# Optimization experiments

Measured on AMD Instinct MI355X. Metric: run time of the kernel, lower is better.

## Reference

```python
import jax, jax.numpy as jnp
import numpy as np

N_NODES = 100000
N_EDGES = 1600000
IN = 128
HID = 128
EPS = 1e-5


def setup_inputs() -> dict:
    key = jax.random.key(0)
    ks = jax.random.split(key, 20)
    def lin(k, fi, fo):
        return jax.random.normal(k, (fi, fo), dtype=jnp.float32) / np.sqrt(fi)
    inp = {
        'x': jax.random.normal(ks[0], (N_NODES, IN), dtype=jnp.float32),
        'src': jax.random.randint(ks[1], (N_EDGES,), 0, N_NODES),
        'dst': jax.random.randint(ks[2], (N_EDGES,), 0, N_NODES),
        # SAGEConv layer 1..3: fc_self, fc_neigh, bias
        'Wself1': lin(ks[3], IN, HID), 'Wneigh1': lin(ks[4], IN, HID), 'b1': jnp.zeros((HID,), jnp.float32),
        'Wself2': lin(ks[5], HID, HID), 'Wneigh2': lin(ks[6], HID, HID), 'b2': jnp.zeros((HID,), jnp.float32),
        'Wself3': lin(ks[7], HID, HID), 'Wneigh3': lin(ks[8], HID, HID), 'b3': jnp.zeros((HID,), jnp.float32),
        # shared BatchNorm1d(hid)
        'gamma': jnp.ones((HID,), jnp.float32), 'beta': jnp.zeros((HID,), jnp.float32),
        # decoder MLP hid->hid->hid->1
        'Wd1': lin(ks[9], HID, HID), 'bd1': jnp.zeros((HID,), jnp.float32),
        'Wd2': lin(ks[10], HID, HID), 'bd2': jnp.zeros((HID,), jnp.float32),
        'Wd3': lin(ks[11], HID, 1), 'bd3': jnp.zeros((1,), jnp.float32),
    }
    return inp


def _sage_conv(h, src, dst, deg, Wself, Wneigh, b, n):
    # mean aggregation over in-neighbors: gather + segment-sum + divide
    neigh_sum = jax.ops.segment_sum(h[src], dst, num_segments=n)  # [N, F]
    neigh_mean = neigh_sum / deg[:, None]
    return h @ Wself + neigh_mean @ Wneigh + b


def _batch_norm(h, gamma, beta):
    mu = jnp.mean(h, axis=0)
    var = jnp.mean(jnp.square(h - mu), axis=0)  # biased var, as torch BN training
    return gamma * (h - mu) * jax.lax.rsqrt(var + EPS) + beta


def reference(x, src, dst, Wself1, Wneigh1, b1, Wself2, Wneigh2, b2,
              Wself3, Wneigh3, b3, gamma, beta, Wd1, bd1, Wd2, bd2, Wd3, bd3):
    n = x.shape[0]
    deg = jax.ops.segment_sum(jnp.ones_like(dst, dtype=x.dtype), dst, num_segments=n)
    deg = jnp.maximum(deg, 1.0)
    h = _sage_conv(x, src, dst, deg, Wself1, Wneigh1, b1, n)
    h = jax.nn.relu(_batch_norm(h, gamma, beta))  # dropout = identity (eval)
    h = _sage_conv(h, src, dst, deg, Wself2, Wneigh2, b2, n)
    h = jax.nn.relu(_batch_norm(h, gamma, beta))
    h = _sage_conv(h, src, dst, deg, Wself3, Wneigh3, b3, n)
    # decoder MLP
    h = jax.nn.relu(h @ Wd1 + bd1)
    h = jax.nn.relu(h @ Wd2 + bd2)
    return h @ Wd3 + bd3  # [N, 1]
```

## Files before the change

### kernel.cpp

```cpp
#include <hip/hip_runtime.h>

typedef unsigned short u16;
typedef unsigned int u32;
using bf16x8 = __attribute__((ext_vector_type(8))) __bf16;
using f32x4  = __attribute__((ext_vector_type(4))) float;

#define CAP 48

__global__ void SAGE_79328045957727_kernel() {}

__device__ __forceinline__ float bf2f(u16 u) {
  union { u32 i; float f; } v; v.i = ((u32)u) << 16; return v.f;
}
__device__ __forceinline__ u16 f2bf(float f) {
  union { float f; u32 i; } v; v.f = f;
  u32 x = v.i;
  return (u16)((x + 0x7FFFu + ((x >> 16) & 1u)) >> 16);
}


__global__ void zero_kernel(int* p, int n) {
  int i = blockIdx.x * 256 + threadIdx.x;
  if (i < n) p[i] = 0;
}

__global__ void f32_to_bf16_kernel(const float* in, u16* out, long n) {
  long i = (long)blockIdx.x * 256 + threadIdx.x;
  if (i < n) out[i] = f2bf(in[i]);
}

__global__ void transpose_all_kernel(
    const float* w0, const float* w1, const float* w2, const float* w3,
    const float* w4, const float* w5, const float* w6, const float* w7,
    u16* wt) {
  int m = blockIdx.x >> 6;
  const float* W = m == 0 ? w0 : m == 1 ? w1 : m == 2 ? w2 : m == 3 ? w3
                 : m == 4 ? w4 : m == 5 ? w5 : m == 6 ? w6 : w7;
  u16* Wt = wt + (size_t)m * 16384;
  int i = (blockIdx.x & 63) * 256 + threadIdx.x;
  int r = i >> 7, c = i & 127;
  Wt[(size_t)c * 128 + r] = f2bf(W[(size_t)r * 128 + c]);
}


__global__ __launch_bounds__(256) void scatter_pad_kernel(
    const int* __restrict__ src, const int* __restrict__ dst,
    int* __restrict__ deg, int* __restrict__ csr, int E, int npart) {
  int p = blockIdx.x & 7;
  int brank = blockIdx.x >> 3;
  int bpp = gridDim.x >> 3;
  int lo = p * npart, hi = lo + npart;
  for (int i = brank * 256 + threadIdx.x; i < E; i += bpp * 256) {
    int dv = dst[i];
    if (dv >= lo && dv < hi) {
      int pos = atomicAdd(&deg[dv], 1);
      if (pos < CAP) csr[(size_t)dv * CAP + pos] = src[i];
    }
  }
}


__global__ __launch_bounds__(256) void gather_mean_kernel(
    const u16* __restrict__ H, const int* __restrict__ csr,
    const int* __restrict__ deg, u16* __restrict__ M, int N) {
  int node = blockIdx.x * 16 + (threadIdx.x >> 4);
  if (node >= N) return;
  int lane = threadIdx.x & 15;
  int fo = lane * 8;
  const int* nl = csr + (size_t)node * CAP;
  int d = deg[node];
  int dm = d < CAP ? d : CAP;
  float a0=0.f,a1=0.f,a2=0.f,a3=0.f,a4=0.f,a5=0.f,a6=0.f,a7=0.f;
  int e = 0;
  for (; e + 4 <= dm; e += 4) {
    int i0 = nl[e];
    int i1 = nl[e + 1];
    int i2 = nl[e + 2];
    int i3 = nl[e + 3];
    uint4 q0 = *(const uint4*)(H + (size_t)i0 * 128 + fo);
    uint4 q1 = *(const uint4*)(H + (size_t)i1 * 128 + fo);
    uint4 q2 = *(const uint4*)(H + (size_t)i2 * 128 + fo);
    uint4 q3 = *(const uint4*)(H + (size_t)i3 * 128 + fo);
    a0 += bf2f((u16)(q0.x & 0xffffu)); a1 += bf2f((u16)(q0.x >> 16));
    a2 += bf2f((u16)(q0.y & 0xffffu)); a3 += bf2f((u16)(q0.y >> 16));
    a4 += bf2f((u16)(q0.z & 0xffffu)); a5 += bf2f((u16)(q0.z >> 16));
    a6 += bf2f((u16)(q0.w & 0xffffu)); a7 += bf2f((u16)(q0.w >> 16));
    a0 += bf2f((u16)(q1.x & 0xffffu)); a1 += bf2f((u16)(q1.x >> 16));
    a2 += bf2f((u16)(q1.y & 0xffffu)); a3 += bf2f((u16)(q1.y >> 16));
    a4 += bf2f((u16)(q1.z & 0xffffu)); a5 += bf2f((u16)(q1.z >> 16));
    a6 += bf2f((u16)(q1.w & 0xffffu)); a7 += bf2f((u16)(q1.w >> 16));
    a0 += bf2f((u16)(q2.x & 0xffffu)); a1 += bf2f((u16)(q2.x >> 16));
    a2 += bf2f((u16)(q2.y & 0xffffu)); a3 += bf2f((u16)(q2.y >> 16));
    a4 += bf2f((u16)(q2.z & 0xffffu)); a5 += bf2f((u16)(q2.z >> 16));
    a6 += bf2f((u16)(q2.w & 0xffffu)); a7 += bf2f((u16)(q2.w >> 16));
    a0 += bf2f((u16)(q3.x & 0xffffu)); a1 += bf2f((u16)(q3.x >> 16));
    a2 += bf2f((u16)(q3.y & 0xffffu)); a3 += bf2f((u16)(q3.y >> 16));
    a4 += bf2f((u16)(q3.z & 0xffffu)); a5 += bf2f((u16)(q3.z >> 16));
    a6 += bf2f((u16)(q3.w & 0xffffu)); a7 += bf2f((u16)(q3.w >> 16));
  }
  for (; e < dm; ++e) {
    int s = nl[e];
    uint4 q = *(const uint4*)(H + (size_t)s * 128 + fo);
    a0 += bf2f((u16)(q.x & 0xffffu)); a1 += bf2f((u16)(q.x >> 16));
    a2 += bf2f((u16)(q.y & 0xffffu)); a3 += bf2f((u16)(q.y >> 16));
    a4 += bf2f((u16)(q.z & 0xffffu)); a5 += bf2f((u16)(q.z >> 16));
    a6 += bf2f((u16)(q.w & 0xffffu)); a7 += bf2f((u16)(q.w >> 16));
  }
  float inv = 1.f / (float)(d > 0 ? d : 1);
  uint4 o;
  o.x = ((u32)f2bf(a1 * inv) << 16) | (u32)f2bf(a0 * inv);
  o.y = ((u32)f2bf(a3 * inv) << 16) | (u32)f2bf(a2 * inv);
  o.z = ((u32)f2bf(a5 * inv) << 16) | (u32)f2bf(a4 * inv);
  o.w = ((u32)f2bf(a7 * inv) << 16) | (u32)f2bf(a6 * inv);
  *(uint4*)(M + (size_t)node * 128 + fo) = o;
}


#define LDSROW 136

template <int DUAL, int RELU, int STATS>
__global__ __launch_bounds__(256) void gemm_mfma(
    const u16* __restrict__ A, const u16* __restrict__ B,
    const u16* __restrict__ W1t, const u16* __restrict__ W2t,
    const float* __restrict__ bias, u16* __restrict__ C,
    float* __restrict__ stats, int N) {
  __shared__ u16 sT[128 * LDSROW];

  int tid = threadIdx.x;
  int wave = tid >> 6;
  int lane = tid & 63;
  int l15 = lane & 15;
  int quad = lane >> 4;
  size_t row0 = (size_t)blockIdx.x * 128;

  f32x4 acc[8][2];
  for (int rt = 0; rt < 8; ++rt)
    for (int ct = 0; ct < 2; ++ct)
      for (int i = 0; i < 4; ++i) acc[rt][ct][i] = 0.f;

  bf16x8 wf[2][4];

  for (int ph = 0; ph < (DUAL ? 2 : 1); ++ph) {
    const u16* Asrc = ph ? B : A;
    const u16* Wt = ph ? W2t : W1t;

    for (int ct = 0; ct < 2; ++ct) {
      int col = wave * 32 + ct * 16 + l15;
      for (int kk = 0; kk < 4; ++kk)
        wf[ct][kk] = *(const bf16x8*)(Wt + (size_t)col * 128 + kk * 32 + quad * 8);
    }

    if (ph) __syncthreads();
    for (int j = 0; j < 8; ++j) {
      int idx = j * 1024 + tid * 4;
      int r = idx >> 6;
      int c = idx & 63;
      size_t grow = row0 + r;
      if (grow >= (size_t)N) grow = (size_t)(N - 1);
      const u32* gp = (const u32*)(Asrc + grow * 128) + c;
      u32 v0 = gp[0], v1 = gp[1], v2 = gp[2], v3 = gp[3];
      u32* lp = (u32*)(sT + (size_t)r * LDSROW + c * 2);
      lp[0] = v0; lp[1] = v1; lp[2] = v2; lp[3] = v3;
    }
    __syncthreads();

    for (int kk = 0; kk < 4; ++kk) {
      int kbase = kk * 32 + quad * 8;
      for (int rt = 0; rt < 8; ++rt) {
        bf16x8 af = *(const bf16x8*)(sT + (size_t)(rt * 16 + l15) * LDSROW + kbase);
        acc[rt][0] = __builtin_amdgcn_mfma_f32_16x16x32_bf16(af, wf[0][kk], acc[rt][0], 0, 0, 0);
        acc[rt][1] = __builtin_amdgcn_mfma_f32_16x16x32_bf16(af, wf[1][kk], acc[rt][1], 0, 0, 0);
      }
    }
  }

  for (int ct = 0; ct < 2; ++ct) {
    int col = wave * 32 + ct * 16 + l15;
    float bv = bias[col];
    float ssum = 0.f, ssq = 0.f;
    for (int rt = 0; rt < 8; ++rt) {
      for (int i = 0; i < 4; ++i) {
        size_t row = row0 + rt * 16 + quad * 4 + i;
        if (row < (size_t)N) {
          float v = acc[rt][ct][i] + bv;
          if (RELU) v = fmaxf(v, 0.f);
          C[row * 128 + col] = f2bf(v);
          if (STATS) { ssum += v; ssq += v * v; }
        }
      }
    }
    if (STATS) {
      for (int o = 16; o < 64; o <<= 1) {
        ssum += __shfl_xor(ssum, o);
        ssq  += __shfl_xor(ssq, o);
      }
      if (quad == 0) {
        atomicAdd(&stats[col], ssum);
        atomicAdd(&stats[128 + col], ssq);
      }
    }
  }
}


__global__ __launch_bounds__(256) void bn_apply_kernel(
    const u16* Z, const float* stats, const float* gamma, const float* beta,
    u16* Hout, int N, float invN) {
  long i = (long)blockIdx.x * 256 + threadIdx.x;
  if (i >= (long)N * 64) return;
  int p = (int)(i & 63);
  float mu0 = stats[p * 2] * invN, mu1 = stats[p * 2 + 1] * invN;
  float var0 = stats[128 + p * 2] * invN - mu0 * mu0;
  float var1 = stats[128 + p * 2 + 1] * invN - mu1 * mu1;
  float is0 = rsqrtf(var0 + 1e-5f), is1 = rsqrtf(var1 + 1e-5f);
  float g0 = gamma[p * 2], g1 = gamma[p * 2 + 1];
  float be0 = beta[p * 2], be1 = beta[p * 2 + 1];
  u32 pr = ((const u32*)Z)[i];
  float z0 = bf2f((u16)(pr & 0xffffu)), z1 = bf2f((u16)(pr >> 16));
  float h0 = fmaxf(g0 * (z0 - mu0) * is0 + be0, 0.f);
  float h1 = fmaxf(g1 * (z1 - mu1) * is1 + be1, 0.f);
  ((u32*)Hout)[i] = ((u32)f2bf(h1) << 16) | (u32)f2bf(h0);
}


__global__ __launch_bounds__(256) void gemv_kernel(
    const u16* Hm, const float* w, const float* b, float* out, int N) {
  int wid = blockIdx.x * 4 + (threadIdx.x >> 6);
  if (wid >= N) return;
  int lane = threadIdx.x & 63;
  u32 p = *(const u32*)(Hm + (size_t)wid * 128 + lane * 2);
  float acc = bf2f((u16)(p & 0xffffu)) * w[lane * 2] +
              bf2f((u16)(p >> 16)) * w[lane * 2 + 1];
  for (int o = 32; o > 0; o >>= 1) acc += __shfl_down(acc, o);
  if (lane == 0) out[wid] = acc + b[0];
}


extern "C" void kernel_launch(void* const* d_in, const int* in_sizes, int n_in,
                              void* d_out, int out_size, void* d_ws, size_t ws_size,
                              hipStream_t stream) {
  const float* x      = (const float*)d_in[0];
  const int*   src    = (const int*)d_in[1];
  const int*   dst    = (const int*)d_in[2];
  const float* Wself1 = (const float*)d_in[3];
  const float* Wneigh1= (const float*)d_in[4];
  const float* b1     = (const float*)d_in[5];
  const float* Wself2 = (const float*)d_in[6];
  const float* Wneigh2= (const float*)d_in[7];
  const float* b2     = (const float*)d_in[8];
  const float* Wself3 = (const float*)d_in[9];
  const float* Wneigh3= (const float*)d_in[10];
  const float* b3     = (const float*)d_in[11];
  const float* gamma  = (const float*)d_in[12];
  const float* beta   = (const float*)d_in[13];
  const float* Wd1    = (const float*)d_in[14];
  const float* bd1    = (const float*)d_in[15];
  const float* Wd2    = (const float*)d_in[16];
  const float* bd2    = (const float*)d_in[17];
  const float* Wd3    = (const float*)d_in[18];
  const float* bd3    = (const float*)d_in[19];
  float* out = (float*)d_out;

  int N = in_sizes[0] / 128;
  int E = in_sizes[1];
  int npart = (N + 7) / 8;

  char* ws = (char*)d_ws;
  size_t off = 0;
  int* deg; int* csr; float* stats1; float* stats2;
  u16* xb; u16* Z; u16* H; u16* M; u16* wt;
  deg   = (int*)(ws + off);   off += (size_t)N * 4;
  stats1= (float*)(ws + off); off += 256 * 4;
  stats2= (float*)(ws + off); off += 256 * 4;
  off = (off + 511) & ~(size_t)511;
  csr  = (int*)(ws + off);   off += ((size_t)N * CAP * 4 + 511) & ~(size_t)511;
  wt   = (u16*)(ws + off);   off += ((size_t)8 * 16384 * 2 + 511) & ~(size_t)511;
  xb   = (u16*)(ws + off);   off += ((size_t)N * 128 * 2 + 511) & ~(size_t)511;
  Z    = (u16*)(ws + off);   off += ((size_t)N * 128 * 2 + 511) & ~(size_t)511;
  H    = (u16*)(ws + off);   off += ((size_t)N * 128 * 2 + 511) & ~(size_t)511;
  M    = (u16*)(ws + off);   off += ((size_t)N * 128 * 2 + 511) & ~(size_t)511;

  u16* wtS1 = wt + 0 * 16384; u16* wtN1 = wt + 1 * 16384;
  u16* wtS2 = wt + 2 * 16384; u16* wtN2 = wt + 3 * 16384;
  u16* wtS3 = wt + 4 * 16384; u16* wtN3 = wt + 5 * 16384;
  u16* wtD1 = wt + 6 * 16384; u16* wtD2 = wt + 7 * 16384;

  zero_kernel<<<(N + 512 + 255) / 256, 256, 0, stream>>>(deg, N + 512);
  scatter_pad_kernel<<<1024, 256, 0, stream>>>(src, dst, deg, csr, E, npart);

  long nelem = (long)N * 128;
  f32_to_bf16_kernel<<<(int)((nelem + 255) / 256), 256, 0, stream>>>(x, xb, nelem);
  transpose_all_kernel<<<512, 256, 0, stream>>>(
      Wself1, Wneigh1, Wself2, Wneigh2, Wself3, Wneigh3, Wd1, Wd2, wt);

  int strips  = (N + 127) / 128;
  int g16     = (N + 15) / 16;
  int gblocks = (N + 3) / 4;
  int eltb    = (int)(((long)N * 64 + 255) / 256);
  float invN  = 1.f / (float)N;

  gather_mean_kernel<<<g16, 256, 0, stream>>>(xb, csr, deg, M, N);
  gemm_mfma<1, 0, 1><<<strips, 256, 0, stream>>>(xb, M, wtS1, wtN1, b1, Z, stats1, N);
  bn_apply_kernel<<<eltb, 256, 0, stream>>>(Z, stats1, gamma, beta, H, N, invN);

  gather_mean_kernel<<<g16, 256, 0, stream>>>(H, csr, deg, M, N);
  gemm_mfma<1, 0, 1><<<strips, 256, 0, stream>>>(H, M, wtS2, wtN2, b2, Z, stats2, N);
  bn_apply_kernel<<<eltb, 256, 0, stream>>>(Z, stats2, gamma, beta, H, N, invN);

  gather_mean_kernel<<<g16, 256, 0, stream>>>(H, csr, deg, M, N);
  gemm_mfma<1, 0, 0><<<strips, 256, 0, stream>>>(H, M, wtS3, wtN3, b3, Z, (float*)0, N);

  gemm_mfma<0, 1, 0><<<strips, 256, 0, stream>>>(Z, (const u16*)0, wtD1, (const u16*)0, bd1, H, (float*)0, N);
  gemm_mfma<0, 1, 0><<<strips, 256, 0, stream>>>(H, (const u16*)0, wtD2, (const u16*)0, bd2, M, (float*)0, N);
  gemv_kernel<<<gblocks, 256, 0, stream>>>(M, Wd3, bd3, out, N);
}
```

Baseline: 645.0 us.

## Fuse batchnorm into gather/GEMM loads, fold final GEMV, merge setup kernels

```diff
diff --git a/kernel.cpp b/kernel.cpp
--- a/kernel.cpp
+++ b/kernel.cpp
@@ -24,88 +24,110 @@
   if (i < n) p[i] = 0;
 }
 
-__global__ void f32_to_bf16_kernel(const float* in, u16* out, long n) {
-  long i = (long)blockIdx.x * 256 + threadIdx.x;
-  if (i < n) out[i] = f2bf(in[i]);
-}
-
-__global__ void transpose_all_kernel(
+
+__global__ __launch_bounds__(256) void build_kernel(
+    const int* __restrict__ src, const int* __restrict__ dst,
+    int* __restrict__ deg, int* __restrict__ csr, int E, int npart,
+    const float* __restrict__ x, u16* __restrict__ xb, long nelem4,
     const float* w0, const float* w1, const float* w2, const float* w3,
     const float* w4, const float* w5, const float* w6, const float* w7,
-    u16* wt) {
-  int m = blockIdx.x >> 6;
-  const float* W = m == 0 ? w0 : m == 1 ? w1 : m == 2 ? w2 : m == 3 ? w3
-                 : m == 4 ? w4 : m == 5 ? w5 : m == 6 ? w6 : w7;
-  u16* Wt = wt + (size_t)m * 16384;
-  int i = (blockIdx.x & 63) * 256 + threadIdx.x;
-  int r = i >> 7, c = i & 127;
-  Wt[(size_t)c * 128 + r] = f2bf(W[(size_t)r * 128 + c]);
-}
-
-
-__global__ __launch_bounds__(256) void scatter_pad_kernel(
-    const int* __restrict__ src, const int* __restrict__ dst,
-    int* __restrict__ deg, int* __restrict__ csr, int E, int npart) {
-  int p = blockIdx.x & 7;
-  int brank = blockIdx.x >> 3;
-  int bpp = gridDim.x >> 3;
-  int lo = p * npart, hi = lo + npart;
-  for (int i = brank * 256 + threadIdx.x; i < E; i += bpp * 256) {
-    int dv = dst[i];
-    if (dv >= lo && dv < hi) {
-      int pos = atomicAdd(&deg[dv], 1);
-      if (pos < CAP) csr[(size_t)dv * CAP + pos] = src[i];
-    }
-  }
-}
-
-
+    u16* __restrict__ wt) {
+  int b = blockIdx.x;
+  if (b < 1024) {
+    int p = b & 7;
+    int brank = b >> 3;
+    int lo = p * npart, hi = lo + npart;
+    for (int i = brank * 256 + threadIdx.x; i < E; i += 128 * 256) {
+      int dv = dst[i];
+      if (dv >= lo && dv < hi) {
+        int pos = atomicAdd(&deg[dv], 1);
+        if (pos < CAP) csr[(size_t)dv * CAP + pos] = src[i];
+      }
+    }
+  } else if (b < 1280) {
+    long t = (long)(b - 1024) * 256 + threadIdx.x;
+    for (long i4 = t; i4 < nelem4; i4 += 256 * 256) {
+      float4 v = ((const float4*)x)[i4];
+      u32* op = (u32*)(xb + i4 * 4);
+      op[0] = ((u32)f2bf(v.y) << 16) | (u32)f2bf(v.x);
+      op[1] = ((u32)f2bf(v.w) << 16) | (u32)f2bf(v.z);
+    }
+  } else {
+    int tg = (b - 1280) * 256 + threadIdx.x;
+    for (int k = 0; k < 8; ++k) {
+      int idx = tg + k * 16384;
+      int m = idx >> 14;
+      int i = idx & 16383;
+      const float* W = m == 0 ? w0 : m == 1 ? w1 : m == 2 ? w2 : m == 3 ? w3
+                     : m == 4 ? w4 : m == 5 ? w5 : m == 6 ? w6 : w7;
+      int r = i >> 7, c = i & 127;
+      wt[(size_t)m * 16384 + (size_t)c * 128 + r] = f2bf(W[i]);
+    }
+  }
+}
+
+
+template <int BNIN>
 __global__ __launch_bounds__(256) void gather_mean_kernel(
     const u16* __restrict__ H, const int* __restrict__ csr,
-    const int* __restrict__ deg, u16* __restrict__ M, int N) {
+    const int* __restrict__ deg, const float* __restrict__ stats,
+    const float* __restrict__ gamma, const float* __restrict__ beta,
+    u16* __restrict__ M, int N, float invN) {
+  __shared__ float sSc[128], sSh[128];
+  if (BNIN) {
+    int t = threadIdx.x;
+    if (t < 128) {
+      float mu = stats[t] * invN;
+      float var = stats[128 + t] * invN - mu * mu;
+      float is = rsqrtf(var + 1e-5f);
+      float sc = gamma[t] * is;
+      sSc[t] = sc;
+      sSh[t] = beta[t] - mu * sc;
+    }
+    __syncthreads();
+  }
   int node = blockIdx.x * 16 + (threadIdx.x >> 4);
   if (node >= N) return;
   int lane = threadIdx.x & 15;
   int fo = lane * 8;
+  float sc[8], sh[8];
+  if (BNIN) {
+    for (int j = 0; j < 8; ++j) { sc[j] = sSc[fo + j]; sh[j] = sSh[fo + j]; }
+  }
   const int* nl = csr + (size_t)node * CAP;
   int d = deg[node];
   int dm = d < CAP ? d : CAP;
   float a0=0.f,a1=0.f,a2=0.f,a3=0.f,a4=0.f,a5=0.f,a6=0.f,a7=0.f;
+
+#define ACCQ(q) do { \
+    float e0 = bf2f((u16)((q).x & 0xffffu)), e1 = bf2f((u16)((q).x >> 16)); \
+    float e2 = bf2f((u16)((q).y & 0xffffu)), e3 = bf2f((u16)((q).y >> 16)); \
+    float e4 = bf2f((u16)((q).z & 0xffffu)), e5 = bf2f((u16)((q).z >> 16)); \
+    float e6 = bf2f((u16)((q).w & 0xffffu)), e7 = bf2f((u16)((q).w >> 16)); \
+    if (BNIN) { \
+      e0 = fmaxf(sc[0]*e0+sh[0], 0.f); e1 = fmaxf(sc[1]*e1+sh[1], 0.f); \
+      e2 = fmaxf(sc[2]*e2+sh[2], 0.f); e3 = fmaxf(sc[3]*e3+sh[3], 0.f); \
+      e4 = fmaxf(sc[4]*e4+sh[4], 0.f); e5 = fmaxf(sc[5]*e5+sh[5], 0.f); \
+      e6 = fmaxf(sc[6]*e6+sh[6], 0.f); e7 = fmaxf(sc[7]*e7+sh[7], 0.f); \
+    } \
+    a0 += e0; a1 += e1; a2 += e2; a3 += e3; \
+    a4 += e4; a5 += e5; a6 += e6; a7 += e7; \
+  } while (0)
+
   int e = 0;
   for (; e + 4 <= dm; e += 4) {
-    int i0 = nl[e];
-    int i1 = nl[e + 1];
-    int i2 = nl[e + 2];
-    int i3 = nl[e + 3];
+    int i0 = nl[e], i1 = nl[e + 1], i2 = nl[e + 2], i3 = nl[e + 3];
     uint4 q0 = *(const uint4*)(H + (size_t)i0 * 128 + fo);
     uint4 q1 = *(const uint4*)(H + (size_t)i1 * 128 + fo);
     uint4 q2 = *(const uint4*)(H + (size_t)i2 * 128 + fo);
     uint4 q3 = *(const uint4*)(H + (size_t)i3 * 128 + fo);
-    a0 += bf2f((u16)(q0.x & 0xffffu)); a1 += bf2f((u16)(q0.x >> 16));
-    a2 += bf2f((u16)(q0.y & 0xffffu)); a3 += bf2f((u16)(q0.y >> 16));
-    a4 += bf2f((u16)(q0.z & 0xffffu)); a5 += bf2f((u16)(q0.z >> 16));
-    a6 += bf2f((u16)(q0.w & 0xffffu)); a7 += bf2f((u16)(q0.w >> 16));
-    a0 += bf2f((u16)(q1.x & 0xffffu)); a1 += bf2f((u16)(q1.x >> 16));
-    a2 += bf2f((u16)(q1.y & 0xffffu)); a3 += bf2f((u16)(q1.y >> 16));
-    a4 += bf2f((u16)(q1.z & 0xffffu)); a5 += bf2f((u16)(q1.z >> 16));
-    a6 += bf2f((u16)(q1.w & 0xffffu)); a7 += bf2f((u16)(q1.w >> 16));
-    a0 += bf2f((u16)(q2.x & 0xffffu)); a1 += bf2f((u16)(q2.x >> 16));
-    a2 += bf2f((u16)(q2.y & 0xffffu)); a3 += bf2f((u16)(q2.y >> 16));
-    a4 += bf2f((u16)(q2.z & 0xffffu)); a5 += bf2f((u16)(q2.z >> 16));
-    a6 += bf2f((u16)(q2.w & 0xffffu)); a7 += bf2f((u16)(q2.w >> 16));
-    a0 += bf2f((u16)(q3.x & 0xffffu)); a1 += bf2f((u16)(q3.x >> 16));
-    a2 += bf2f((u16)(q3.y & 0xffffu)); a3 += bf2f((u16)(q3.y >> 16));
-    a4 += bf2f((u16)(q3.z & 0xffffu)); a5 += bf2f((u16)(q3.z >> 16));
-    a6 += bf2f((u16)(q3.w & 0xffffu)); a7 += bf2f((u16)(q3.w >> 16));
+    ACCQ(q0); ACCQ(q1); ACCQ(q2); ACCQ(q3);
   }
   for (; e < dm; ++e) {
-    int s = nl[e];
-    uint4 q = *(const uint4*)(H + (size_t)s * 128 + fo);
-    a0 += bf2f((u16)(q.x & 0xffffu)); a1 += bf2f((u16)(q.x >> 16));
-    a2 += bf2f((u16)(q.y & 0xffffu)); a3 += bf2f((u16)(q.y >> 16));
-    a4 += bf2f((u16)(q.z & 0xffffu)); a5 += bf2f((u16)(q.z >> 16));
-    a6 += bf2f((u16)(q.w & 0xffffu)); a7 += bf2f((u16)(q.w >> 16));
-  }
+    uint4 q = *(const uint4*)(H + (size_t)nl[e] * 128 + fo);
+    ACCQ(q);
+  }
+#undef ACCQ
   float inv = 1.f / (float)(d > 0 ? d : 1);
   uint4 o;
   o.x = ((u32)f2bf(a1 * inv) << 16) | (u32)f2bf(a0 * inv);
@@ -118,13 +140,18 @@
 
 #define LDSROW 136
 
-template <int DUAL, int RELU, int STATS>
+template <int DUAL, int RELU, int STATS, int BNIN, int FINAL>
 __global__ __launch_bounds__(256) void gemm_mfma(
     const u16* __restrict__ A, const u16* __restrict__ B,
     const u16* __restrict__ W1t, const u16* __restrict__ W2t,
     const float* __restrict__ bias, u16* __restrict__ C,
-    float* __restrict__ stats, int N) {
+    float* __restrict__ statsOut, const float* __restrict__ statsIn,
+    const float* __restrict__ gamma, const float* __restrict__ beta,
+    const float* __restrict__ wd3, const float* __restrict__ bd3,
+    float* __restrict__ outF, int N, float invN) {
   __shared__ u16 sT[128 * LDSROW];
+  __shared__ float sSc[128], sSh[128];
+  __shared__ float sOut[128];
 
   int tid = threadIdx.x;
   int wave = tid >> 6;
@@ -132,6 +159,27 @@
   int l15 = lane & 15;
   int quad = lane >> 4;
   size_t row0 = (size_t)blockIdx.x * 128;
+
+  if (BNIN || FINAL) {
+    if (tid < 128) {
+      if (BNIN) {
+        float mu = statsIn[tid] * invN;
+        float var = statsIn[128 + tid] * invN - mu * mu;
+        float is = rsqrtf(var + 1e-5f);
+        float sc = gamma[tid] * is;
+        sSc[tid] = sc;
+        sSh[tid] = beta[tid] - mu * sc;
+      }
+      if (FINAL) sOut[tid] = 0.f;
+    }
+    __syncthreads();
+  }
+
+  float bsc[8], bsh[8];
+  int cbase = ((tid * 4) & 63) * 2;
+  if (BNIN) {
+    for (int j = 0; j < 8; ++j) { bsc[j] = sSc[cbase + j]; bsh[j] = sSh[cbase + j]; }
+  }
 
   f32x4 acc[8][2];
   for (int rt = 0; rt < 8; ++rt)
@@ -159,6 +207,20 @@
       if (grow >= (size_t)N) grow = (size_t)(N - 1);
       const u32* gp = (const u32*)(Asrc + grow * 128) + c;
       u32 v0 = gp[0], v1 = gp[1], v2 = gp[2], v3 = gp[3];
+      if (BNIN && ph == 0) {
+        float e0 = fmaxf(bsc[0]*bf2f((u16)(v0 & 0xffffu))+bsh[0], 0.f);
+        float e1 = fmaxf(bsc[1]*bf2f((u16)(v0 >> 16))+bsh[1], 0.f);
+        float e2 = fmaxf(bsc[2]*bf2f((u16)(v1 & 0xffffu))+bsh[2], 0.f);
+        float e3 = fmaxf(bsc[3]*bf2f((u16)(v1 >> 16))+bsh[3], 0.f);
+        float e4 = fmaxf(bsc[4]*bf2f((u16)(v2 & 0xffffu))+bsh[4], 0.f);
+        float e5 = fmaxf(bsc[5]*bf2f((u16)(v2 >> 16))+bsh[5], 0.f);
+        float e6 = fmaxf(bsc[6]*bf2f((u16)(v3 & 0xffffu))+bsh[6], 0.f);
+        float e7 = fmaxf(bsc[7]*bf2f((u16)(v3 >> 16))+bsh[7], 0.f);
+        v0 = ((u32)f2bf(e1) << 16) | (u32)f2bf(e0);
+        v1 = ((u32)f2bf(e3) << 16) | (u32)f2bf(e2);
+        v2 = ((u32)f2bf(e5) << 16) | (u32)f2bf(e4);
+        v3 = ((u32)f2bf(e7) << 16) | (u32)f2bf(e6);
+      }
       u32* lp = (u32*)(sT + (size_t)r * LDSROW + c * 2);
       lp[0] = v0; lp[1] = v1; lp[2] = v2; lp[3] = v3;
     }
@@ -172,6 +234,32 @@
         acc[rt][1] = __builtin_amdgcn_mfma_f32_16x16x32_bf16(af, wf[1][kk], acc[rt][1], 0, 0, 0);
       }
     }
+  }
+
+  if (FINAL) {
+    int col0 = wave * 32 + l15;
+    float bv0 = bias[col0], bv1 = bias[col0 + 16];
+    float w30 = wd3[col0], w31 = wd3[col0 + 16];
+    for (int rt = 0; rt < 8; ++rt) {
+      for (int i = 0; i < 4; ++i) {
+        size_t row = row0 + rt * 16 + quad * 4 + i;
+        float v0 = fmaxf(acc[rt][0][i] + bv0, 0.f);
+        float v1 = fmaxf(acc[rt][1][i] + bv1, 0.f);
+        float pv = v0 * w30 + v1 * w31;
+        pv += __shfl_xor(pv, 1);
+        pv += __shfl_xor(pv, 2);
+        pv += __shfl_xor(pv, 4);
+        pv += __shfl_xor(pv, 8);
+        if (l15 == 0 && row < (size_t)N)
+          atomicAdd(&sOut[rt * 16 + quad * 4 + i], pv);
+      }
+    }
+    __syncthreads();
+    if (tid < 128) {
+      size_t row = row0 + tid;
+      if (row < (size_t)N) outF[row] = sOut[tid] + bd3[0];
+    }
+    return;
   }
 
   for (int ct = 0; ct < 2; ++ct) {
@@ -195,44 +283,11 @@
         ssq  += __shfl_xor(ssq, o);
       }
       if (quad == 0) {
-        atomicAdd(&stats[col], ssum);
-        atomicAdd(&stats[128 + col], ssq);
-      }
-    }
-  }
-}
-
-
-__global__ __launch_bounds__(256) void bn_apply_kernel(
-    const u16* Z, const float* stats, const float* gamma, const float* beta,
-    u16* Hout, int N, float invN) {
-  long i = (long)blockIdx.x * 256 + threadIdx.x;
-  if (i >= (long)N * 64) return;
-  int p = (int)(i & 63);
-  float mu0 = stats[p * 2] * invN, mu1 = stats[p * 2 + 1] * invN;
-  float var0 = stats[128 + p * 2] * invN - mu0 * mu0;
-  float var1 = stats[128 + p * 2 + 1] * invN - mu1 * mu1;
-  float is0 = rsqrtf(var0 + 1e-5f), is1 = rsqrtf(var1 + 1e-5f);
-  float g0 = gamma[p * 2], g1 = gamma[p * 2 + 1];
-  float be0 = beta[p * 2], be1 = beta[p * 2 + 1];
-  u32 pr = ((const u32*)Z)[i];
-  float z0 = bf2f((u16)(pr & 0xffffu)), z1 = bf2f((u16)(pr >> 16));
-  float h0 = fmaxf(g0 * (z0 - mu0) * is0 + be0, 0.f);
-  float h1 = fmaxf(g1 * (z1 - mu1) * is1 + be1, 0.f);
-  ((u32*)Hout)[i] = ((u32)f2bf(h1) << 16) | (u32)f2bf(h0);
-}
-
-
-__global__ __launch_bounds__(256) void gemv_kernel(
-    const u16* Hm, const float* w, const float* b, float* out, int N) {
-  int wid = blockIdx.x * 4 + (threadIdx.x >> 6);
-  if (wid >= N) return;
-  int lane = threadIdx.x & 63;
-  u32 p = *(const u32*)(Hm + (size_t)wid * 128 + lane * 2);
-  float acc = bf2f((u16)(p & 0xffffu)) * w[lane * 2] +
-              bf2f((u16)(p >> 16)) * w[lane * 2 + 1];
-  for (int o = 32; o > 0; o >>= 1) acc += __shfl_down(acc, o);
-  if (lane == 0) out[wid] = acc + b[0];
+        atomicAdd(&statsOut[col], ssum);
+        atomicAdd(&statsOut[128 + col], ssq);
+      }
+    }
+  }
 }
 
 
@@ -268,7 +323,7 @@
   char* ws = (char*)d_ws;
   size_t off = 0;
   int* deg; int* csr; float* stats1; float* stats2;
-  u16* xb; u16* Z; u16* H; u16* M; u16* wt;
+  u16* xb; u16* ZA; u16* ZB; u16* M; u16* wt;
   deg   = (int*)(ws + off);   off += (size_t)N * 4;
   stats1= (float*)(ws + off); off += 256 * 4;
   stats2= (float*)(ws + off); off += 256 * 4;
@@ -276,8 +331,8 @@
   csr  = (int*)(ws + off);   off += ((size_t)N * CAP * 4 + 511) & ~(size_t)511;
   wt   = (u16*)(ws + off);   off += ((size_t)8 * 16384 * 2 + 511) & ~(size_t)511;
   xb   = (u16*)(ws + off);   off += ((size_t)N * 128 * 2 + 511) & ~(size_t)511;
-  Z    = (u16*)(ws + off);   off += ((size_t)N * 128 * 2 + 511) & ~(size_t)511;
-  H    = (u16*)(ws + off);   off += ((size_t)N * 128 * 2 + 511) & ~(size_t)511;
+  ZA   = (u16*)(ws + off);   off += ((size_t)N * 128 * 2 + 511) & ~(size_t)511;
+  ZB   = (u16*)(ws + off);   off += ((size_t)N * 128 * 2 + 511) & ~(size_t)511;
   M    = (u16*)(ws + off);   off += ((size_t)N * 128 * 2 + 511) & ~(size_t)511;
 
   u16* wtS1 = wt + 0 * 16384; u16* wtN1 = wt + 1 * 16384;
@@ -286,31 +341,38 @@
   u16* wtD1 = wt + 6 * 16384; u16* wtD2 = wt + 7 * 16384;
 
   zero_kernel<<<(N + 512 + 255) / 256, 256, 0, stream>>>(deg, N + 512);
-  scatter_pad_kernel<<<1024, 256, 0, stream>>>(src, dst, deg, csr, E, npart);
-
-  long nelem = (long)N * 128;
-  f32_to_bf16_kernel<<<(int)((nelem + 255) / 256), 256, 0, stream>>>(x, xb, nelem);
-  transpose_all_kernel<<<512, 256, 0, stream>>>(
+
+  long nelem4 = (long)N * 128 / 4;
+  build_kernel<<<1344, 256, 0, stream>>>(
+      src, dst, deg, csr, E, npart, x, xb, nelem4,
       Wself1, Wneigh1, Wself2, Wneigh2, Wself3, Wneigh3, Wd1, Wd2, wt);
 
-  int strips  = (N + 127) / 128;
-  int g16     = (N + 15) / 16;
-  int gblocks = (N + 3) / 4;
-  int eltb    = (int)(((long)N * 64 + 255) / 256);
-  float invN  = 1.f / (float)N;
-
-  gather_mean_kernel<<<g16, 256, 0, stream>>>(xb, csr, deg, M, N);
-  gemm_mfma<1, 0, 1><<<strips, 256, 0, stream>>>(xb, M, wtS1, wtN1, b1, Z, stats1, N);
-  bn_apply_kernel<<<eltb, 256, 0, stream>>>(Z, stats1, gamma, beta, H, N, invN);
-
-  gather_mean_kernel<<<g16, 256, 0, stream>>>(H, csr, deg, M, N);
-  gemm_mfma<1, 0, 1><<<strips, 256, 0, stream>>>(H, M, wtS2, wtN2, b2, Z, stats2, N);
-  bn_apply_kernel<<<eltb, 256, 0, stream>>>(Z, stats2, gamma, beta, H, N, invN);
-
-  gather_mean_kernel<<<g16, 256, 0, stream>>>(H, csr, deg, M, N);
-  gemm_mfma<1, 0, 0><<<strips, 256, 0, stream>>>(H, M, wtS3, wtN3, b3, Z, (float*)0, N);
-
-  gemm_mfma<0, 1, 0><<<strips, 256, 0, stream>>>(Z, (const u16*)0, wtD1, (const u16*)0, bd1, H, (float*)0, N);
-  gemm_mfma<0, 1, 0><<<strips, 256, 0, stream>>>(H, (const u16*)0, wtD2, (const u16*)0, bd2, M, (float*)0, N);
-  gemv_kernel<<<gblocks, 256, 0, stream>>>(M, Wd3, bd3, out, N);
-}
+  int strips = (N + 127) / 128;
+  int g16    = (N + 15) / 16;
+  float invN = 1.f / (float)N;
+
+  gather_mean_kernel<0><<<g16, 256, 0, stream>>>(
+      xb, csr, deg, (const float*)0, (const float*)0, (const float*)0, M, N, invN);
+  gemm_mfma<1, 0, 1, 0, 0><<<strips, 256, 0, stream>>>(
+      xb, M, wtS1, wtN1, b1, ZA, stats1, (const float*)0, (const float*)0,
+      (const float*)0, (const float*)0, (const float*)0, (float*)0, N, invN);
+
+  gather_mean_kernel<1><<<g16, 256, 0, stream>>>(
+      ZA, csr, deg, stats1, gamma, beta, M, N, invN);
+  gemm_mfma<1, 0, 1, 1, 0><<<strips, 256, 0, stream>>>(
+      ZA, M, wtS2, wtN2, b2, ZB, stats2, stats1, gamma, beta,
+      (const float*)0, (const float*)0, (float*)0, N, invN);
+
+  gather_mean_kernel<1><<<g16, 256, 0, stream>>>(
+      ZB, csr, deg, stats2, gamma, beta, M, N, invN);
+  gemm_mfma<1, 0, 0, 1, 0><<<strips, 256, 0, stream>>>(
+      ZB, M, wtS3, wtN3, b3, ZA, (float*)0, stats2, gamma, beta,
+      (const float*)0, (const float*)0, (float*)0, N, invN);
+
+  gemm_mfma<0, 1, 0, 0, 0><<<strips, 256, 0, stream>>>(
+      ZA, (const u16*)0, wtD1, (const u16*)0, bd1, ZB, (float*)0, (const float*)0,
+      (const float*)0, (const float*)0, (const float*)0, (const float*)0, (float*)0, N, invN);
+  gemm_mfma<0, 1, 0, 0, 1><<<strips, 256, 0, stream>>>(
+      ZB, (const u16*)0, wtD2, (const u16*)0, bd2, (u16*)0, (float*)0, (const float*)0,
+      (const float*)0, (const float*)0, Wd3, bd3, out, N, invN);
+}
```

After: 598.1 us. 7.3% less time.
